# Performance work log

Hardware: AMD Instinct MI355X
Metric: run time of the kernel (lower is better)

## Reference

```python
import jax, jax.numpy as jnp
import numpy as np
import math

BLOCK_SIZE = 64
GATE_HIDDEN = 128


def _rmsnorm(x, w, eps=1e-6):
    v = jnp.mean(jnp.square(x), axis=-1, keepdims=True)
    return x * jax.lax.rsqrt(v + eps) * w


def _rotate_half(x):
    x1, x2 = jnp.split(x, 2, axis=-1)
    return jnp.concatenate([-x2, x1], axis=-1)


def _rope(x, cos, sin):
    # x: [B, S, H, D]; cos/sin: [B, S, D] -> unsqueeze head dim (unsqueeze_dim=2)
    c = cos[:, :, None, :]
    s = sin[:, :, None, :]
    return x * c + _rotate_half(x) * s


def setup_inputs() -> dict:
    key = jax.random.key(0)
    ks = jax.random.split(key, 10)
    B, S, Hk, D = 4, 65536, 8, 128
    Hq, g, Dg = 32, 4, GATE_HIDDEN
    nb = S // BLOCK_SIZE
    xav_q = math.sqrt(6.0 / (D + Dg))
    xav_k = math.sqrt(6.0 / (2 * D + Dg))
    return {
        "k": jax.random.normal(ks[0], (B, S, Hk, D), jnp.float32),
        "q": jax.random.normal(ks[1], (B, 1, Hq, D), jnp.float32),
        "Wq": jax.random.uniform(ks[2], (Hk, g, D, Dg), jnp.float32, -xav_q, xav_q),
        "Wk": jax.random.uniform(ks[3], (Hk, 2 * D, Dg), jnp.float32, -xav_k, xav_k),
        "qnorm_w": jnp.ones((Dg,), jnp.float32),
        "knorm_w": jnp.ones((Dg,), jnp.float32),
        "cos_q": jax.random.uniform(ks[4], (B, 1, Dg), jnp.float32, -1.0, 1.0),
        "sin_q": jax.random.uniform(ks[5], (B, 1, Dg), jnp.float32, -1.0, 1.0),
        "cos_k": jax.random.uniform(ks[6], (B, nb, Dg), jnp.float32, -1.0, 1.0),
        "sin_k": jax.random.uniform(ks[7], (B, nb, Dg), jnp.float32, -1.0, 1.0),
        "attention_mask": jnp.ones((B, Hk, nb), jnp.bool_),
        "block_budget": 128,
    }


def reference(k, q, Wq, Wk, qnorm_w, knorm_w, cos_q, sin_q, cos_k, sin_k,
              attention_mask, block_budget):
    B, S, Hk, D = k.shape
    nb = S // BLOCK_SIZE
    g = q.shape[2] // Hk
    Dg = Wk.shape[-1]
    scale = 1.0 / math.sqrt(Dg)

    # --- K path: block pooling (avg + max) -> per-head linear -> RMSNorm -> RoPE
    kb = k.reshape(B, nb, BLOCK_SIZE, Hk, D)
    k_pooled = jnp.concatenate([kb.mean(axis=2), kb.max(axis=2)], axis=-1)  # [B,nb,Hk,2D]
    k_c = jnp.einsum('bshi,hio->bsho', k_pooled, Wk)                         # [B,nb,Hk,Dg]
    k_c = _rmsnorm(k_c, knorm_w)
    k_c = _rope(k_c, cos_k, sin_k)

    # --- Q path (Qproj): grouped per-k-head projection -> RMSNorm -> RoPE
    qg = q.reshape(B, 1, Hk, g, D)
    qp = jnp.einsum('bskgi,kgio->bsko', qg, Wq)                              # [B,1,Hk,Dg]
    qp = _rmsnorm(qp, qnorm_w)
    qp = _rope(qp, cos_q, sin_q)
    qv = qp[:, 0]                                                            # [B,Hk,Dg]

    # --- gate scores + softmax
    attn = jnp.einsum('bhd,bshd->bhs', qv, k_c) * scale                      # [B,Hk,nb]
    attn = jnp.where(attention_mask, attn, jnp.float32(-1e20))
    attn = jax.nn.softmax(attn, axis=-1)

    # --- token_budget sparse block mask: topk + scatter
    _, topk_idx = jax.lax.top_k(attn, block_budget)                          # [B,Hk,k]
    blk = jnp.arange(nb)
    mask = jnp.any(topk_idx[..., :, None] == blk[None, None, None, :], axis=-2)
    mask = mask & attention_mask
    mask = mask.at[:, :, -1].set(True)
    return mask
```

## Files before the change

### kernel.cpp

```cpp
#include <hip/hip_runtime.h>
#include <hip/hip_bf16.h>
#include <math.h>

#define NB   1024
#define HKH  8
#define NPROD 512
#define NCONS 256

typedef float f4 __attribute__((ext_vector_type(4)));

__global__ __launch_bounds__(512) void qproj_kernel(const float* __restrict__ q,
                                                    const float* __restrict__ Wq,
                                                    const float* __restrict__ qnw,
                                                    const float* __restrict__ cq,
                                                    const float* __restrict__ sq,
                                                    float* __restrict__ qv) {
    int b = blockIdx.x >> 3, h = blockIdx.x & 7;
    int t = threadIdx.x;
    int o = t & 127, seg = t >> 7;
    __shared__ float qs[512];
    __shared__ float part[4][128];
    __shared__ float red[2];
    __shared__ float ybuf[128];
    qs[t] = q[(size_t)b * 4096 + (size_t)h * 512 + t];
    __syncthreads();
    const float* wqp = Wq + (size_t)h * 512 * 128 + o;
    float acc = 0.0f;
    int g0 = seg * 128;
#pragma unroll 4
    for (int gi = g0; gi < g0 + 128; ++gi)
        acc = fmaf(qs[gi], wqp[(size_t)gi * 128], acc);
    part[seg][o] = acc;
    __syncthreads();
    if (t < 128) {
        float a = part[0][o] + part[1][o] + part[2][o] + part[3][o];
        ybuf[o] = a;
        float ss = a * a;
        for (int off = 32; off > 0; off >>= 1) ss += __shfl_xor(ss, off);
        if ((o & 63) == 0) red[o >> 6] = ss;
    }
    __syncthreads();
    if (t < 128) {
        float scale = rsqrtf((red[0] + red[1]) * (1.0f / 128.0f) + 1e-6f);
        float y  = ybuf[o] * scale * qnw[o];
        int op   = (o < 64) ? o + 64 : o - 64;
        float yp = ybuf[op] * scale * qnw[op];
        float rot = (o < 64) ? -yp : yp;
        qv[((size_t)b * HKH + h) * 128 + o] =
            fmaf(y, cq[b * 128 + o], rot * sq[b * 128 + o]);
    }
}

__global__ __launch_bounds__(768) void fused_kernel(const float* __restrict__ kin,
                                                    const float* __restrict__ Wk,
                                                    const float* __restrict__ knw,
                                                    const float* __restrict__ cosk,
                                                    const float* __restrict__ sink,
                                                    const float* __restrict__ qv,
                                                    float* __restrict__ scores) {
    __shared__ float At[4][256][32];
    __shared__ int produced[4];
    int wg  = blockIdx.x;
    int b   = wg >> 6;
    int grp = wg & 63;
    int t   = threadIdx.x;

    if (t < 4) produced[t] = 0;
    __syncthreads();

    if (t < NPROD) {
        int col = t & 255;
        int h   = col >> 5;
        int c   = col & 31;
        int bihalf = t >> 8;
        const float inv = 1.0f / 64.0f;
        for (int it = 0; it < 4; ++it) {
#pragma unroll
            for (int bb2 = 0; bb2 < 2; ++bb2) {
                int bi = bihalf + bb2 * 2;
                size_t row0 = (size_t)b * 65536 +
                              ((size_t)grp * 16 + it * 4 + bi) * 64;
                const f4* src = (const f4*)kin + row0 * 256 + col;
                f4 s = {0.f, 0.f, 0.f, 0.f};
                f4 m = {-3.4e38f, -3.4e38f, -3.4e38f, -3.4e38f};
#pragma unroll 8
                for (int r = 0; r < 64; ++r) {
                    f4 u = __builtin_nontemporal_load(src + (size_t)r * 256);
                    s += u;
                    m.x = fmaxf(m.x, u.x); m.y = fmaxf(m.y, u.y);
                    m.z = fmaxf(m.z, u.z); m.w = fmaxf(m.w, u.w);
                }
#pragma unroll
                for (int j = 0; j < 4; ++j) {
                    int k0 = c * 4 + j;
                    int g  = (k0 >> 3) & 7;
                    At[it][k0      ][((h ^ g) << 2) | bi] = s[j] * inv;
                    At[it][k0 + 128][((h ^ g) << 2) | bi] = m[j];
                }
            }
            __threadfence_block();
            atomicAdd(&produced[it], 1);
        }
    } else {
        int tc = t - NPROD;
        int h  = tc >> 5;
        int c  = tc & 31;
        const float* wp = Wk + (size_t)h * 32768 + c * 4;
        f4 kn  = *(const f4*)(knw + c * 4);
        f4 qvr = *(const f4*)(qv + ((size_t)b * HKH + h) * 128 + c * 4);
        volatile int* vfl = (volatile int*)produced;

        for (int it = 0; it < 4; ++it) {
            while (vfl[it] < NPROD) __builtin_amdgcn_s_sleep(2);
            __threadfence_block();

            float acc[4][4];
#pragma unroll
            for (int i = 0; i < 4; ++i)
#pragma unroll
                for (int j = 0; j < 4; ++j) acc[i][j] = 0.0f;
#pragma unroll 4
            for (int k = 0; k < 256; ++k) {
                int g = (k >> 3) & 7;
                f4 a = *(const f4*)&At[it][k][(h ^ g) << 2];
                f4 w = *(const f4*)(wp + (size_t)k * 128);
#pragma unroll
                for (int i = 0; i < 4; ++i) {
                    acc[i][0] = fmaf(a[i], w.x, acc[i][0]);
                    acc[i][1] = fmaf(a[i], w.y, acc[i][1]);
                    acc[i][2] = fmaf(a[i], w.z, acc[i][2]);
                    acc[i][3] = fmaf(a[i], w.w, acc[i][3]);
                }
            }

#pragma unroll
            for (int i = 0; i < 4; ++i) {
                int blkg = (grp * 16 + it * 4) + i;
                float ss = 0.0f;
#pragma unroll
                for (int j = 0; j < 4; ++j) ss = fmaf(acc[i][j], acc[i][j], ss);
#pragma unroll
                for (int off = 1; off < 32; off <<= 1) ss += __shfl_xor(ss, off);
                float scale = rsqrtf(ss * (1.0f / 128.0f) + 1e-6f);
                f4 cb = *(const f4*)(cosk + ((size_t)b * NB + blkg) * 128 + c * 4);
                f4 sb = *(const f4*)(sink + ((size_t)b * NB + blkg) * 128 + c * 4);
                float part = 0.0f;
#pragma unroll
                for (int j = 0; j < 4; ++j) {
                    float y  = acc[i][j] * scale * kn[j];
                    float yp = __shfl_xor(y, 16);
                    float rot = (c < 16) ? -yp : yp;
                    float z = fmaf(y, cb[j], rot * sb[j]);
                    part = fmaf(z, qvr[j], part);
                }
#pragma unroll
                for (int off = 1; off < 32; off <<= 1) part += __shfl_xor(part, off);
                if (c == 0)
                    scores[((size_t)b * HKH + h) * NB + blkg] =
                        part * 0.08838834764831845f;
            }
        }
    }
}

__device__ inline bool read_mask(const void* amp, int mode, size_t idx) {
    if (mode == 1) return ((const int*)amp)[idx] != 0;
    if (mode == 2) return ((const unsigned int*)amp)[idx] != 0u;
    return ((const unsigned char*)amp)[idx] != 0;
}

__global__ __launch_bounds__(512) void topk_kernel(const float* __restrict__ scores,
                                                   const void* __restrict__ amraw,
                                                   const int* __restrict__ bbp,
                                                   int* __restrict__ out) {
    int b = blockIdx.x >> 3, h = blockIdx.x & 7;
    int t = threadIdx.x;
    __shared__ float sv[NB];
    __shared__ int mode_sh;

    if (t == 0) {
        const unsigned int* w = (const unsigned int*)amraw;
        bool allint = true, allflt = true;
        for (int i = 0; i < 64; ++i) {
            unsigned int x = w[i];
            if (x != 0u && x != 1u) allint = false;
            if (x != 0u && x != 0x3f800000u) allflt = false;
        }
        mode_sh = allint ? 1 : (allflt ? 2 : 0);
    }
    __syncthreads();
    int mode = mode_sh;
    size_t rowoff = ((size_t)b * HKH + h) * NB;
    const float* src = scores + rowoff;
    for (int s = t; s < NB; s += 512)
        sv[s] = read_mask(amraw, mode, rowoff + s) ? src[s] : -1e20f;
    __syncthreads();

    int bb = bbp[0];
    if (bb > NB) bb = NB;
    if (bb < 1)  bb = 1;

    int e0 = t, e1 = t + 512;
    float v0 = sv[e0], v1 = sv[e1];
    int r0 = 0, r1 = 0;
#pragma unroll 4
    for (int j4 = 0; j4 < 256; ++j4) {
        f4 w = *(const f4*)&sv[j4 * 4];
        int jb = j4 * 4;
        r0 += (w.x > v0) + (w.y > v0) + (w.z > v0) + (w.w > v0);
        r1 += (w.x > v1) + (w.y > v1) + (w.z > v1) + (w.w > v1);
        r0 += (w.x == v0 && jb + 0 < e0) + (w.y == v0 && jb + 1 < e0)
            + (w.z == v0 && jb + 2 < e0) + (w.w == v0 && jb + 3 < e0);
        r1 += (w.x == v1 && jb + 0 < e1) + (w.y == v1 && jb + 1 < e1)
            + (w.z == v1 && jb + 2 < e1) + (w.w == v1 && jb + 3 < e1);
    }
    int* dst = out + rowoff;
    bool am0 = read_mask(amraw, mode, rowoff + e0);
    bool am1 = read_mask(amraw, mode, rowoff + e1);
    dst[e0] = ((r0 < bb && am0)) ? 1 : 0;
    dst[e1] = ((r1 < bb && am1) || (e1 == NB - 1)) ? 1 : 0;
}

extern "C" void kernel_launch(void* const* d_in, const int* in_sizes, int n_in,
                              void* d_out, int out_size, void* d_ws, size_t ws_size,
                              hipStream_t stream) {
    (void)in_sizes; (void)n_in; (void)out_size; (void)ws_size;
    const float* k   = (const float*)d_in[0];
    const float* q   = (const float*)d_in[1];
    const float* Wq  = (const float*)d_in[2];
    const float* Wk  = (const float*)d_in[3];
    const float* qnw = (const float*)d_in[4];
    const float* knw = (const float*)d_in[5];
    const float* cq  = (const float*)d_in[6];
    const float* sq  = (const float*)d_in[7];
    const float* ck  = (const float*)d_in[8];
    const float* sk  = (const float*)d_in[9];
    const void*  am  = d_in[10];
    const int*   bb  = (const int*)d_in[11];
    int* out = (int*)d_out;

    float* qv     = (float*)d_ws;
    float* scores = qv + 4 * HKH * 128;

    qproj_kernel<<<32, 512, 0, stream>>>(q, Wq, qnw, cq, sq, qv);
    fused_kernel<<<256, 768, 0, stream>>>(k, Wk, knw, ck, sk, qv, scores);
    topk_kernel<<<32, 512, 0, stream>>>(scores, am, bb, out);
}
```

Measured before the change: 262.3 us.

## Fuse Q projection into consumer warps and interleave two block loads in producers

Removes the separate qproj kernel launch; each consumer thread now computes its four outputs of the grouped Q projection, RMSNorm (via a 32-lane shuffle reduction) and RoPE (via an xor-16 shuffle) while the producers pool K. The producer loop now loads two pooling blocks per iteration instead of running them back to back, and drops the nontemporal load hint. This saves a launch and its global round trip, and is meant to hide the Q projection behind the K streaming. In exchange the Wq reads are repeated in every one of the 64 workgroups per batch, and removing the nontemporal hint may change how the K stream interacts with the caches.

```diff
diff --git a/kernel.cpp b/kernel.cpp
--- a/kernel.cpp
+++ b/kernel.cpp
@@ -5,58 +5,19 @@
 #define NB   1024
 #define HKH  8
 #define NPROD 512
-#define NCONS 256
 
 typedef float f4 __attribute__((ext_vector_type(4)));
 
-__global__ __launch_bounds__(512) void qproj_kernel(const float* __restrict__ q,
+__global__ __launch_bounds__(768) void fused_kernel(const float* __restrict__ kin,
+                                                    const float* __restrict__ qrow,
                                                     const float* __restrict__ Wq,
+                                                    const float* __restrict__ Wk,
                                                     const float* __restrict__ qnw,
+                                                    const float* __restrict__ knw,
                                                     const float* __restrict__ cq,
                                                     const float* __restrict__ sq,
-                                                    float* __restrict__ qv) {
-    int b = blockIdx.x >> 3, h = blockIdx.x & 7;
-    int t = threadIdx.x;
-    int o = t & 127, seg = t >> 7;
-    __shared__ float qs[512];
-    __shared__ float part[4][128];
-    __shared__ float red[2];
-    __shared__ float ybuf[128];
-    qs[t] = q[(size_t)b * 4096 + (size_t)h * 512 + t];
-    __syncthreads();
-    const float* wqp = Wq + (size_t)h * 512 * 128 + o;
-    float acc = 0.0f;
-    int g0 = seg * 128;
-#pragma unroll 4
-    for (int gi = g0; gi < g0 + 128; ++gi)
-        acc = fmaf(qs[gi], wqp[(size_t)gi * 128], acc);
-    part[seg][o] = acc;
-    __syncthreads();
-    if (t < 128) {
-        float a = part[0][o] + part[1][o] + part[2][o] + part[3][o];
-        ybuf[o] = a;
-        float ss = a * a;
-        for (int off = 32; off > 0; off >>= 1) ss += __shfl_xor(ss, off);
-        if ((o & 63) == 0) red[o >> 6] = ss;
-    }
-    __syncthreads();
-    if (t < 128) {
-        float scale = rsqrtf((red[0] + red[1]) * (1.0f / 128.0f) + 1e-6f);
-        float y  = ybuf[o] * scale * qnw[o];
-        int op   = (o < 64) ? o + 64 : o - 64;
-        float yp = ybuf[op] * scale * qnw[op];
-        float rot = (o < 64) ? -yp : yp;
-        qv[((size_t)b * HKH + h) * 128 + o] =
-            fmaf(y, cq[b * 128 + o], rot * sq[b * 128 + o]);
-    }
-}
-
-__global__ __launch_bounds__(768) void fused_kernel(const float* __restrict__ kin,
-                                                    const float* __restrict__ Wk,
-                                                    const float* __restrict__ knw,
                                                     const float* __restrict__ cosk,
                                                     const float* __restrict__ sink,
-                                                    const float* __restrict__ qv,
                                                     float* __restrict__ scores) {
     __shared__ float At[4][256][32];
     __shared__ int produced[4];
@@ -75,28 +36,32 @@
         int bihalf = t >> 8;
         const float inv = 1.0f / 64.0f;
         for (int it = 0; it < 4; ++it) {
-#pragma unroll
-            for (int bb2 = 0; bb2 < 2; ++bb2) {
-                int bi = bihalf + bb2 * 2;
-                size_t row0 = (size_t)b * 65536 +
-                              ((size_t)grp * 16 + it * 4 + bi) * 64;
-                const f4* src = (const f4*)kin + row0 * 256 + col;
-                f4 s = {0.f, 0.f, 0.f, 0.f};
-                f4 m = {-3.4e38f, -3.4e38f, -3.4e38f, -3.4e38f};
-#pragma unroll 8
-                for (int r = 0; r < 64; ++r) {
-                    f4 u = __builtin_nontemporal_load(src + (size_t)r * 256);
-                    s += u;
-                    m.x = fmaxf(m.x, u.x); m.y = fmaxf(m.y, u.y);
-                    m.z = fmaxf(m.z, u.z); m.w = fmaxf(m.w, u.w);
-                }
-#pragma unroll
-                for (int j = 0; j < 4; ++j) {
-                    int k0 = c * 4 + j;
-                    int g  = (k0 >> 3) & 7;
-                    At[it][k0      ][((h ^ g) << 2) | bi] = s[j] * inv;
-                    At[it][k0 + 128][((h ^ g) << 2) | bi] = m[j];
-                }
+            size_t rbase = (size_t)b * 65536 + ((size_t)grp * 16 + it * 4) * 64;
+            int bi0 = bihalf, bi1 = bihalf + 2;
+            const f4* srcA = (const f4*)kin + (rbase + (size_t)bi0 * 64) * 256 + col;
+            const f4* srcB = (const f4*)kin + (rbase + (size_t)bi1 * 64) * 256 + col;
+            f4 sA = {0.f, 0.f, 0.f, 0.f}, sB = {0.f, 0.f, 0.f, 0.f};
+            f4 mA = {-3.4e38f, -3.4e38f, -3.4e38f, -3.4e38f};
+            f4 mB = mA;
+#pragma unroll 4
+            for (int r = 0; r < 64; ++r) {
+                f4 uA = srcA[(size_t)r * 256];
+                f4 uB = srcB[(size_t)r * 256];
+                sA += uA;
+                mA.x = fmaxf(mA.x, uA.x); mA.y = fmaxf(mA.y, uA.y);
+                mA.z = fmaxf(mA.z, uA.z); mA.w = fmaxf(mA.w, uA.w);
+                sB += uB;
+                mB.x = fmaxf(mB.x, uB.x); mB.y = fmaxf(mB.y, uB.y);
+                mB.z = fmaxf(mB.z, uB.z); mB.w = fmaxf(mB.w, uB.w);
+            }
+#pragma unroll
+            for (int j = 0; j < 4; ++j) {
+                int k0 = c * 4 + j;
+                int g  = (k0 >> 3) & 7;
+                At[it][k0      ][((h ^ g) << 2) | bi0] = sA[j] * inv;
+                At[it][k0 + 128][((h ^ g) << 2) | bi0] = mA[j];
+                At[it][k0      ][((h ^ g) << 2) | bi1] = sB[j] * inv;
+                At[it][k0 + 128][((h ^ g) << 2) | bi1] = mB[j];
             }
             __threadfence_block();
             atomicAdd(&produced[it], 1);
@@ -105,9 +70,35 @@
         int tc = t - NPROD;
         int h  = tc >> 5;
         int c  = tc & 31;
+
+        f4 qvr;
+        {
+            const float* qsrc = qrow + (size_t)b * 4096 + (size_t)h * 512;
+            const f4* wqp = (const f4*)(Wq + (size_t)h * 65536) + c;
+            f4 aq = {0.f, 0.f, 0.f, 0.f};
+#pragma unroll 8
+            for (int gi = 0; gi < 512; ++gi) {
+                f4 w = wqp[(size_t)gi * 32];
+                float qg = qsrc[gi];
+                aq.x = fmaf(qg, w.x, aq.x); aq.y = fmaf(qg, w.y, aq.y);
+                aq.z = fmaf(qg, w.z, aq.z); aq.w = fmaf(qg, w.w, aq.w);
+            }
+            float ss = aq.x*aq.x + aq.y*aq.y + aq.z*aq.z + aq.w*aq.w;
+#pragma unroll
+            for (int off = 1; off < 32; off <<= 1) ss += __shfl_xor(ss, off);
+            float scale = rsqrtf(ss * (1.0f / 128.0f) + 1e-6f);
+#pragma unroll
+            for (int j = 0; j < 4; ++j) {
+                int o = c * 4 + j;
+                float y  = aq[j] * scale * qnw[o];
+                float yp = __shfl_xor(y, 16);
+                float rot = (c < 16) ? -yp : yp;
+                qvr[j] = fmaf(y, cq[b * 128 + o], rot * sq[b * 128 + o]);
+            }
+        }
+
         const float* wp = Wk + (size_t)h * 32768 + c * 4;
-        f4 kn  = *(const f4*)(knw + c * 4);
-        f4 qvr = *(const f4*)(qv + ((size_t)b * HKH + h) * 128 + c * 4);
+        f4 kn = *(const f4*)(knw + c * 4);
         volatile int* vfl = (volatile int*)produced;
 
         for (int it = 0; it < 4; ++it) {
@@ -239,10 +230,9 @@
     const int*   bb  = (const int*)d_in[11];
     int* out = (int*)d_out;
 
-    float* qv     = (float*)d_ws;
-    float* scores = qv + 4 * HKH * 128;
-
-    qproj_kernel<<<32, 512, 0, stream>>>(q, Wq, qnw, cq, sq, qv);
-    fused_kernel<<<256, 768, 0, stream>>>(k, Wk, knw, ck, sk, qv, scores);
+    float* scores = (float*)d_ws;
+
+    fused_kernel<<<256, 768, 0, stream>>>(k, q, Wq, Wk, qnw, knw,
+                                          cq, sq, ck, sk, scores);
     topk_kernel<<<32, 512, 0, stream>>>(scores, am, bb, out);
 }
```

Result: slower. 328.1 us (+25.1%).
